# Performance work log

Hardware: AMD Instinct MI355X
Metric: run time of the kernel (lower is better)

The kernel has to match this reference:

```python
import jax, jax.numpy as jnp
import numpy as np

N = 20000      # nodes
E = 640000     # edges (before self-loops)
F = 64         # base node feature len
H = 2          # heads per layer
EPS = 1e-5
NEG_SLOPE = 0.2  # PyG GATConv leaky_relu slope


def setup_inputs():
    key = jax.random.key(0)
    ks = jax.random.split(key, 16)
    s = 0.1
    x = jax.random.normal(ks[0], (N, F), jnp.float32)
    edge_index = jax.random.randint(ks[1], (2, E), 0, N, dtype=jnp.int64)
    # layer 1: in=F, heads=H, out-per-head C1=F -> out dim H*F=128
    C1 = F
    W1 = jax.random.normal(ks[2], (F, H * C1), jnp.float32) * s
    att_src1 = jax.random.normal(ks[3], (H, C1), jnp.float32) * s
    att_dst1 = jax.random.normal(ks[4], (H, C1), jnp.float32) * s
    bias1 = jnp.zeros((H * C1,), jnp.float32)
    gamma1 = jnp.ones((H * C1,), jnp.float32)
    beta1 = jnp.zeros((H * C1,), jnp.float32)
    # layer 2: in=H*F=128, heads=H, out-per-head C2=H*F -> out dim H*H*F=256
    C2 = H * F
    W2 = jax.random.normal(ks[5], (H * C1, H * C2), jnp.float32) * s
    att_src2 = jax.random.normal(ks[6], (H, C2), jnp.float32) * s
    att_dst2 = jax.random.normal(ks[7], (H, C2), jnp.float32) * s
    bias2 = jnp.zeros((H * C2,), jnp.float32)
    gamma2 = jnp.ones((H * C2,), jnp.float32)
    beta2 = jnp.zeros((H * C2,), jnp.float32)
    return {"x": x, "edge_index": edge_index,
            "W1": W1, "att_src1": att_src1, "att_dst1": att_dst1, "bias1": bias1,
            "gamma1": gamma1, "beta1": beta1,
            "W2": W2, "att_src2": att_src2, "att_dst2": att_dst2, "bias2": bias2,
            "gamma2": gamma2, "beta2": beta2}


def _gat_conv(x, src, dst, W, att_src, att_dst, bias):
    # PyG GATConv (concat=True, add_self_loops already applied to src/dst)
    n = x.shape[0]
    h, c = att_src.shape
    hx = (x @ W).reshape(n, h, c)                       # [N,H,C]
    a_s = jnp.einsum('nhc,hc->nh', hx, att_src)         # [N,H]
    a_d = jnp.einsum('nhc,hc->nh', hx, att_dst)
    e = a_s[src] + a_d[dst]                             # [E',H]
    e = jnp.where(e > 0, e, NEG_SLOPE * e)              # leaky relu
    # segment softmax over incoming edges of each target node
    m = jax.ops.segment_max(e, dst, num_segments=n)     # [N,H]
    p = jnp.exp(e - m[dst])
    z = jax.ops.segment_sum(p, dst, num_segments=n)     # [N,H]
    alpha = p / z[dst]                                  # [E',H]
    msg = hx[src] * alpha[:, :, None]                   # [E',H,C]
    out = jax.ops.segment_sum(msg, dst, num_segments=n) # [N,H,C]
    return out.reshape(n, h * c) + bias


def _batch_norm(x, gamma, beta):
    mu = x.mean(axis=0)
    var = x.var(axis=0)  # biased, matches torch BN normalization
    return (x - mu) * jax.lax.rsqrt(var + EPS) * gamma + beta


def reference(x, edge_index, W1, att_src1, att_dst1, bias1, gamma1, beta1,
              W2, att_src2, att_dst2, bias2, gamma2, beta2):
    loops = jnp.arange(N, dtype=edge_index.dtype)
    src = jnp.concatenate([edge_index[0], loops])
    dst = jnp.concatenate([edge_index[1], loops])
    h = _gat_conv(x, src, dst, W1, att_src1, att_dst1, bias1)
    h = jax.nn.relu(_batch_norm(h, gamma1, beta1))
    h = _gat_conv(h, src, dst, W2, att_src2, att_dst2, bias2)
    h = jax.nn.relu(_batch_norm(h, gamma2, beta2))
    return h
```

## Files before the change

kernel.cpp:

```cpp
#include <hip/hip_runtime.h>
#include <hip/hip_bf16.h>
#include <math.h>

#define NN 20000
#define ER 640000
#define ET 660000
#define D1 128
#define D2 256
#define EPSV 1e-5f
#define SLOPE 0.2f
#define NT1 313
#define NHIST 64
#define HCH 10000

typedef __attribute__((ext_vector_type(8))) short bf16x8;
typedef __attribute__((ext_vector_type(4))) float f32x4;

__device__ __forceinline__ int detect64(const void* ei) {
  const int* p = (const int*)ei;
  return (p[1] | p[3] | p[5] | p[7]) == 0;
}
__device__ __forceinline__ int clampn(int v) { return v < 0 ? 0 : (v >= NN ? NN-1 : v); }
__device__ __forceinline__ float bf16_lo(unsigned int u){ return __uint_as_float(u<<16); }
__device__ __forceinline__ float bf16_hi(unsigned int u){ return __uint_as_float(u & 0xffff0000u); }

__global__ void k_hist(const void* ei, unsigned int* dpart, int* gcount) {
  extern __shared__ unsigned int hist[];
  int db = blockIdx.x, t = threadIdx.x;
  if (db == 0 && t == 0) *gcount = 0;
  for (int i = t; i < HCH; i += 256) hist[i] = 0;
  __syncthreads();
  int base = db * HCH;
  if (detect64(ei)) {
    const long long* q = (const long long*)ei + ER;
    for (int i = base + t; i < base + HCH; i += 256) {
      int d = clampn((int)q[i]);
      atomicAdd(&hist[d>>1], 1u << ((d&1)*16));
    }
  } else {
    const int* q = (const int*)ei + ER;
    for (int i = base + t; i < base + HCH; i += 256) {
      int d = clampn(q[i]);
      atomicAdd(&hist[d>>1], 1u << ((d&1)*16));
    }
  }
  __syncthreads();
  for (int i = t; i < HCH; i += 256) dpart[(size_t)db*HCH + i] = hist[i];
}

__global__ __launch_bounds__(256) void k_alloc(const unsigned int* dpart, int* begv, int* endv,
                                               int* cursor, int* gcount, float* bnz) {
  __shared__ int wsum[4], wbase[4];
  int gid = blockIdx.x*256 + threadIdx.x;
  if (gid < 768) bnz[gid] = 0.f;
  int d = 0;
  if (gid < NN) {
    d = 1;
    int half = (gid & 1) * 16;
    int idx = gid >> 1;
    for (int db = 0; db < NHIST; db++)
      d += (dpart[(size_t)db*HCH + idx] >> half) & 0xffff;
  }
  int lane = threadIdx.x & 63, w = threadIdx.x >> 6;
  int v = d;
  #pragma unroll
  for (int o = 1; o < 64; o <<= 1) {
    int u = __shfl_up(v, o);
    if (lane >= o) v += u;
  }
  if (lane == 63) wsum[w] = v;
  __syncthreads();
  if (threadIdx.x == 0) {
    int s0 = wsum[0], s1 = wsum[1], s2 = wsum[2], s3 = wsum[3];
    int b = atomicAdd(gcount, s0 + s1 + s2 + s3);
    wbase[0] = b; wbase[1] = b + s0; wbase[2] = b + s0 + s1; wbase[3] = b + s0 + s1 + s2;
  }
  __syncthreads();
  if (gid < NN) {
    int beg = wbase[w] + v - d;
    begv[gid] = beg; cursor[gid] = beg; endv[gid] = beg + d;
  }
}

__global__ __launch_bounds__(256) void k_gs(const float* x, const float* W1,
                                            const float* att_s1, const float* att_d1,
                                            __hip_bfloat16* hxb, float2* as1, float2* ad1,
                                            const void* ei, int* cursor, int* srcs) {
  __shared__ __hip_bfloat16 As[64][72];
  __shared__ __hip_bfloat16 Bs[128][72];
  __shared__ float asred[4][64], adred[4][64];
  int b = blockIdx.x, t = threadIdx.x;
  if (b >= NT1) {
    int i0 = ((b - NT1)*256 + t)*4;
    if (i0 >= ET) return;
    int s[4], d[4];
    if (i0 >= ER) {
      #pragma unroll
      for (int k = 0; k < 4; k++) { s[k] = i0 + k - ER; d[k] = s[k]; }
    } else if (detect64(ei)) {
      const long long* p64 = (const long long*)ei;
      uint4 qa = *(const uint4*)(p64 + i0);
      uint4 qb = *(const uint4*)(p64 + i0 + 2);
      uint4 ra = *(const uint4*)(p64 + ER + i0);
      uint4 rb = *(const uint4*)(p64 + ER + i0 + 2);
      s[0]=clampn((int)qa.x); s[1]=clampn((int)qa.z); s[2]=clampn((int)qb.x); s[3]=clampn((int)qb.z);
      d[0]=clampn((int)ra.x); d[1]=clampn((int)ra.z); d[2]=clampn((int)rb.x); d[3]=clampn((int)rb.z);
    } else {
      const int* p32 = (const int*)ei;
      uint4 qs = *(const uint4*)(p32 + i0);
      uint4 qd = *(const uint4*)(p32 + ER + i0);
      s[0]=clampn((int)qs.x); s[1]=clampn((int)qs.y); s[2]=clampn((int)qs.z); s[3]=clampn((int)qs.w);
      d[0]=clampn((int)qd.x); d[1]=clampn((int)qd.y); d[2]=clampn((int)qd.z); d[3]=clampn((int)qd.w);
    }
    #pragma unroll
    for (int k = 0; k < 4; k++) {
      int pos = atomicAdd(&cursor[d[k]], 1);
      srcs[pos] = s[k];
    }
    return;
  }
  int m0 = b * 64;
  for (int i = t; i < 512; i += 256) {
    int r = i >> 3, s = i & 7;
    int gr = m0 + r; if (gr >= NN) gr = NN - 1;
    float4 f0 = ((const float4*)(x + (size_t)gr*64))[s*2];
    float4 f1 = ((const float4*)(x + (size_t)gr*64))[s*2+1];
    __hip_bfloat16 hb[8] = {
      __float2bfloat16(f0.x), __float2bfloat16(f0.y), __float2bfloat16(f0.z), __float2bfloat16(f0.w),
      __float2bfloat16(f1.x), __float2bfloat16(f1.y), __float2bfloat16(f1.z), __float2bfloat16(f1.w)};
    *(uint4*)&As[r][s*8] = *(uint4*)hb;
  }
  for (int i = t; i < 8192; i += 256) {
    int n = i & 127, k = i >> 7;
    Bs[n][k] = __float2bfloat16(W1[k*128 + n]);
  }
  __syncthreads();
  int w = t >> 6, lane = t & 63, lm = lane & 15, q = lane >> 4;
  f32x4 acc[4][2];
  #pragma unroll
  for (int rt = 0; rt < 4; rt++)
    #pragma unroll
    for (int ct = 0; ct < 2; ct++) acc[rt][ct] = (f32x4){0.f,0.f,0.f,0.f};
  #pragma unroll
  for (int kc = 0; kc < 2; kc++) {
    bf16x8 bfr[2];
    #pragma unroll
    for (int ct = 0; ct < 2; ct++)
      bfr[ct] = *(const bf16x8*)&Bs[w*32 + ct*16 + lm][kc*32 + q*8];
    #pragma unroll
    for (int rt = 0; rt < 4; rt++) {
      bf16x8 a = *(const bf16x8*)&As[rt*16 + lm][kc*32 + q*8];
      acc[rt][0] = __builtin_amdgcn_mfma_f32_16x16x32_bf16(a, bfr[0], acc[rt][0], 0, 0, 0);
      acc[rt][1] = __builtin_amdgcn_mfma_f32_16x16x32_bf16(a, bfr[1], acc[rt][1], 0, 0, 0);
    }
  }
  #pragma unroll
  for (int rt = 0; rt < 4; rt++)
    #pragma unroll
    for (int ct = 0; ct < 2; ct++)
      #pragma unroll
      for (int rg = 0; rg < 4; rg++) {
        int row = m0 + rt*16 + q*4 + rg;
        int col = w*32 + ct*16 + lm;
        if (row < NN) hxb[(size_t)row*128 + col] = __float2bfloat16(acc[rt][ct][rg]);
      }
  float asc[2], adc[2];
  #pragma unroll
  for (int ct = 0; ct < 2; ct++) {
    int col = w*32 + ct*16 + lm;
    asc[ct] = att_s1[col]; adc[ct] = att_d1[col];
  }
  #pragma unroll
  for (int rt = 0; rt < 4; rt++)
    #pragma unroll
    for (int rg = 0; rg < 4; rg++) {
      float ps = acc[rt][0][rg]*asc[0] + acc[rt][1][rg]*asc[1];
      float pd = acc[rt][0][rg]*adc[0] + acc[rt][1][rg]*adc[1];
      #pragma unroll
      for (int o = 1; o < 16; o <<= 1) { ps += __shfl_xor(ps, o); pd += __shfl_xor(pd, o); }
      if (lm == 0) { int row = rt*16 + q*4 + rg; asred[w][row] = ps; adred[w][row] = pd; }
    }
  __syncthreads();
  if (t < 64) {
    int row = m0 + t;
    if (row < NN) {
      as1[row] = make_float2(asred[0][t] + asred[1][t], asred[2][t] + asred[3][t]);
      ad1[row] = make_float2(adred[0][t] + adred[1][t], adred[2][t] + adred[3][t]);
    }
  }
}

__global__ __launch_bounds__(256) void k_gemm2f(const float* out1, const float* W2,
                                                const float* bns1, const float* bnq1,
                                                const float* gamma1, const float* beta1,
                                                const float* att_s2, const float* att_d2,
                                                __hip_bfloat16* hxb, float2* as2, float2* ad2) {
  __shared__ __hip_bfloat16 As[64][136];
  __shared__ __hip_bfloat16 Bs[256][40];
  __shared__ float AB[2][128];
  __shared__ float asred[4][64], adred[4][64];
  int t = threadIdx.x;
  int m0 = blockIdx.x * 64;
  if (t < 128) {
    float mean = bns1[t]*(1.f/NN);
    float var  = bnq1[t]*(1.f/NN) - mean*mean;
    float A = rsqrtf(var + EPSV)*gamma1[t];
    AB[0][t] = A; AB[1][t] = beta1[t] - mean*A;
  }
  __syncthreads();
  for (int i = t; i < 1024; i += 256) {
    int r = i >> 4, s = i & 15;
    int gr = m0 + r; if (gr >= NN) gr = NN - 1;
    float4 f0 = ((const float4*)(out1 + (size_t)gr*128))[s*2];
    float4 f1 = ((const float4*)(out1 + (size_t)gr*128))[s*2+1];
    int c = s*8;
    float v[8] = {f0.x,f0.y,f0.z,f0.w,f1.x,f1.y,f1.z,f1.w};
    __hip_bfloat16 hb[8];
    #pragma unroll
    for (int k = 0; k < 8; k++)
      hb[k] = __float2bfloat16(fmaxf(v[k]*AB[0][c+k] + AB[1][c+k], 0.f));
    *(uint4*)&As[r][s*8] = *(uint4*)hb;
  }
  int w = t >> 6, lane = t & 63, lm = lane & 15, q = lane >> 4;
  f32x4 acc[4][4];
  #pragma unroll
  for (int rt = 0; rt < 4; rt++)
    #pragma unroll
    for (int ct = 0; ct < 4; ct++) acc[rt][ct] = (f32x4){0.f,0.f,0.f,0.f};
  for (int kc = 0; kc < 4; kc++) {
    __syncthreads();
    for (int i = t; i < 8192; i += 256) {
      int n = i & 255, kk = i >> 8;
      Bs[n][kk] = __float2bfloat16(W2[(kc*32 + kk)*256 + n]);
    }
    __syncthreads();
    bf16x8 bfr[4];
    #pragma unroll
    for (int ct = 0; ct < 4; ct++)
      bfr[ct] = *(const bf16x8*)&Bs[w*64 + ct*16 + lm][q*8];
    #pragma unroll
    for (int rt = 0; rt < 4; rt++) {
      bf16x8 a = *(const bf16x8*)&As[rt*16 + lm][kc*32 + q*8];
      #pragma unroll
      for (int ct = 0; ct < 4; ct++)
        acc[rt][ct] = __builtin_amdgcn_mfma_f32_16x16x32_bf16(a, bfr[ct], acc[rt][ct], 0, 0, 0);
    }
  }
  #pragma unroll
  for (int rt = 0; rt < 4; rt++)
    #pragma unroll
    for (int ct = 0; ct < 4; ct++)
      #pragma unroll
      for (int rg = 0; rg < 4; rg++) {
        int row = m0 + rt*16 + q*4 + rg;
        int col = w*64 + ct*16 + lm;
        if (row < NN) hxb[(size_t)row*256 + col] = __float2bfloat16(acc[rt][ct][rg]);
      }
  float asc[4], adc[4];
  #pragma unroll
  for (int ct = 0; ct < 4; ct++) {
    int col = w*64 + ct*16 + lm;
    asc[ct] = att_s2[col]; adc[ct] = att_d2[col];
  }
  #pragma unroll
  for (int rt = 0; rt < 4; rt++)
    #pragma unroll
    for (int rg = 0; rg < 4; rg++) {
      float ps = acc[rt][0][rg]*asc[0] + acc[rt][1][rg]*asc[1]
               + acc[rt][2][rg]*asc[2] + acc[rt][3][rg]*asc[3];
      float pd = acc[rt][0][rg]*adc[0] + acc[rt][1][rg]*adc[1]
               + acc[rt][2][rg]*adc[2] + acc[rt][3][rg]*adc[3];
      #pragma unroll
      for (int o = 1; o < 16; o <<= 1) { ps += __shfl_xor(ps, o); pd += __shfl_xor(pd, o); }
      if (lm == 0) { int row = rt*16 + q*4 + rg; asred[w][row] = ps; adred[w][row] = pd; }
    }
  __syncthreads();
  if (t < 64) {
    int row = m0 + t;
    if (row < NN) {
      as2[row] = make_float2(asred[0][t] + asred[1][t], asred[2][t] + asred[3][t]);
      ad2[row] = make_float2(adred[0][t] + adred[1][t], adred[2][t] + adred[3][t]);
    }
  }
}

__global__ __launch_bounds__(64) void k_agg1(const int* begv, const int* endv, const int* srcs,
                                             const float2* asv, const float2* adv,
                                             const uint4* hx, const float* bias, float* out) {
  __shared__ float2 sp[2][64];
  int n = blockIdx.x, t = threadIdx.x;
  int el = t >> 4, c = t & 15;
  int h = c >> 3;
  float2 ad = adv[n];
  int beg = begv[n], end = endv[n];
  float a[8] = {0.f,0.f,0.f,0.f,0.f,0.f,0.f,0.f};
  float z0 = 0.f, z1 = 0.f;
  for (int cb = beg; cb < end; cb += 64) {
    int len = end - cb; if (len > 64) len = 64;
    if (t < len) {
      int s = srcs[cb + t];
      float2 as = asv[s];
      float e0 = as.x + ad.x, e1 = as.y + ad.y;
      e0 = e0 > 0.f ? e0 : SLOPE*e0;
      e1 = e1 > 0.f ? e1 : SLOPE*e1;
      float p0 = __expf(e0), p1 = __expf(e1);
      sp[0][t] = make_float2(__int_as_float(s), p0);
      sp[1][t] = make_float2(__int_as_float(s), p1);
      z0 += p0; z1 += p1;
    }
    __syncthreads();
    for (int j = 0; j < len; j += 4) {
      int e = j + el;
      if (e < len) {
        float2 v = sp[h][e];
        uint4 u = hx[(size_t)__float_as_int(v.x)*16 + c];
        float pj = v.y;
        a[0] += pj*bf16_lo(u.x); a[1] += pj*bf16_hi(u.x);
        a[2] += pj*bf16_lo(u.y); a[3] += pj*bf16_hi(u.y);
        a[4] += pj*bf16_lo(u.z); a[5] += pj*bf16_hi(u.z);
        a[6] += pj*bf16_lo(u.w); a[7] += pj*bf16_hi(u.w);
      }
    }
    __syncthreads();
  }
  #pragma unroll
  for (int k = 0; k < 8; k++) {
    a[k] += __shfl_down(a[k], 32);
    a[k] += __shfl_down(a[k], 16);
  }
  #pragma unroll
  for (int o = 1; o < 64; o <<= 1) { z0 += __shfl_xor(z0, o); z1 += __shfl_xor(z1, o); }
  if (t < 16) {
    float inv = 1.f / (h ? z1 : z0);
    float4 b0 = ((const float4*)bias)[2*c];
    float4 b1 = ((const float4*)bias)[2*c+1];
    float4 o0 = { a[0]*inv + b0.x, a[1]*inv + b0.y, a[2]*inv + b0.z, a[3]*inv + b0.w };
    float4 o1 = { a[4]*inv + b1.x, a[5]*inv + b1.y, a[6]*inv + b1.z, a[7]*inv + b1.w };
    ((float4*)(out + (size_t)n*D1))[2*c]   = o0;
    ((float4*)(out + (size_t)n*D1))[2*c+1] = o1;
  }
}

__global__ __launch_bounds__(64) void k_agg2(const int* begv, const int* endv, const int* srcs,
                                             const float2* asv, const float2* adv,
                                             const uint4* hx, const float* bias, float* out) {
  __shared__ float2 sp[2][64];
  int n = blockIdx.x, t = threadIdx.x;
  int el = t >> 5, c = t & 31;
  int h = c >> 4;
  float2 ad = adv[n];
  int beg = begv[n], end = endv[n];
  float a[8] = {0.f,0.f,0.f,0.f,0.f,0.f,0.f,0.f};
  float z0 = 0.f, z1 = 0.f;
  for (int cb = beg; cb < end; cb += 64) {
    int len = end - cb; if (len > 64) len = 64;
    if (t < len) {
      int s = srcs[cb + t];
      float2 as = asv[s];
      float e0 = as.x + ad.x, e1 = as.y + ad.y;
      e0 = e0 > 0.f ? e0 : SLOPE*e0;
      e1 = e1 > 0.f ? e1 : SLOPE*e1;
      float p0 = __expf(e0), p1 = __expf(e1);
      sp[0][t] = make_float2(__int_as_float(s), p0);
      sp[1][t] = make_float2(__int_as_float(s), p1);
      z0 += p0; z1 += p1;
    }
    __syncthreads();
    for (int j = 0; j < len; j += 2) {
      int e = j + el;
      if (e < len) {
        float2 v = sp[h][e];
        uint4 u = hx[(size_t)__float_as_int(v.x)*32 + c];
        float pj = v.y;
        a[0] += pj*bf16_lo(u.x); a[1] += pj*bf16_hi(u.x);
        a[2] += pj*bf16_lo(u.y); a[3] += pj*bf16_hi(u.y);
        a[4] += pj*bf16_lo(u.z); a[5] += pj*bf16_hi(u.z);
        a[6] += pj*bf16_lo(u.w); a[7] += pj*bf16_hi(u.w);
      }
    }
    __syncthreads();
  }
  #pragma unroll
  for (int k = 0; k < 8; k++) a[k] += __shfl_down(a[k], 32);
  #pragma unroll
  for (int o = 1; o < 64; o <<= 1) { z0 += __shfl_xor(z0, o); z1 += __shfl_xor(z1, o); }
  if (t < 32) {
    float inv = 1.f / (h ? z1 : z0);
    float4 b0 = ((const float4*)bias)[2*c];
    float4 b1 = ((const float4*)bias)[2*c+1];
    float4 o0 = { a[0]*inv + b0.x, a[1]*inv + b0.y, a[2]*inv + b0.z, a[3]*inv + b0.w };
    float4 o1 = { a[4]*inv + b1.x, a[5]*inv + b1.y, a[6]*inv + b1.z, a[7]*inv + b1.w };
    ((float4*)(out + (size_t)n*D2))[2*c]   = o0;
    ((float4*)(out + (size_t)n*D2))[2*c+1] = o1;
  }
}

template<int D>
__global__ void k_bnstats(const float* x, float* bnsum, float* bnsq) {
  const int ROWS = 100;
  int c = threadIdx.x;
  int r0 = blockIdx.x * ROWS;
  float s = 0.f, s2 = 0.f;
  for (int r = 0; r < ROWS; r++) {
    float v = x[(size_t)(r0 + r)*D + c];
    s += v; s2 += v*v;
  }
  atomicAdd(&bnsum[c], s);
  atomicAdd(&bnsq[c], s2);
}

__global__ void k_bnapply2(const float* x, const float* bnsum, const float* bnsq,
                           const float* gamma, const float* beta, float* out) {
  int i = blockIdx.x*blockDim.x + threadIdx.x;
  if (i >= NN*D2/4) return;
  int c = (i & 63) * 4;
  float4 v = ((const float4*)x)[i];
  float r[4] = {v.x, v.y, v.z, v.w};
  #pragma unroll
  for (int k = 0; k < 4; k++) {
    float mean = bnsum[c+k] * (1.f/NN);
    float var  = bnsq[c+k] * (1.f/NN) - mean*mean;
    float o = (r[k] - mean) * rsqrtf(var + EPSV) * gamma[c+k] + beta[c+k];
    r[k] = o > 0.f ? o : 0.f;
  }
  float4 o4 = {r[0], r[1], r[2], r[3]};
  ((float4*)out)[i] = o4;
}

extern "C" void kernel_launch(void* const* d_in, const int* in_sizes, int n_in,
                              void* d_out, int out_size, void* d_ws, size_t ws_size,
                              hipStream_t stream) {
  const float* x      = (const float*)d_in[0];
  const void*  ei     = d_in[1];
  const float* W1     = (const float*)d_in[2];
  const float* att_s1 = (const float*)d_in[3];
  const float* att_d1 = (const float*)d_in[4];
  const float* bias1  = (const float*)d_in[5];
  const float* gamma1 = (const float*)d_in[6];
  const float* beta1  = (const float*)d_in[7];
  const float* W2     = (const float*)d_in[8];
  const float* att_s2 = (const float*)d_in[9];
  const float* att_d2 = (const float*)d_in[10];
  const float* bias2  = (const float*)d_in[11];
  const float* gamma2 = (const float*)d_in[12];
  const float* beta2  = (const float*)d_in[13];

  char* p = (char*)d_ws;
  __hip_bfloat16* hx1b = (__hip_bfloat16*)p; p += (size_t)NN*D1*2;
  __hip_bfloat16* hx2b = (__hip_bfloat16*)p; p += (size_t)NN*D2*2;
  float* out1 = (float*)p; p += (size_t)NN*D1*4;
  float* out2 = (float*)p; p += (size_t)NN*D2*4;
  float2* as1 = (float2*)p; p += (size_t)NN*8;
  float2* ad1 = (float2*)p; p += (size_t)NN*8;
  float2* as2 = (float2*)p; p += (size_t)NN*8;
  float2* ad2 = (float2*)p; p += (size_t)NN*8;
  float* bns1 = (float*)p; p += D1*4;
  float* bnq1 = (float*)p; p += D1*4;
  float* bns2 = (float*)p; p += D2*4;
  float* bnq2 = (float*)p; p += D2*4;
  unsigned int* dpart = (unsigned int*)p; p += (size_t)NHIST*HCH*4;
  int* begv   = (int*)p; p += NN*4;
  int* endv   = (int*)p; p += NN*4;
  int* cursor = (int*)p; p += NN*4;
  int* gcount = (int*)p; p += 16*4;
  int* srcs   = (int*)p; p += (size_t)ET*4;

  const int SCB = (ET/4 + 255)/256;
  k_hist<<<NHIST, 256, HCH*4, stream>>>(ei, dpart, gcount);
  k_alloc<<<(NN+255)/256, 256, 0, stream>>>(dpart, begv, endv, cursor, gcount, bns1);
  k_gs<<<NT1 + SCB, 256, 0, stream>>>(x, W1, att_s1, att_d1, hx1b, as1, ad1,
                                      ei, cursor, srcs);

  k_agg1<<<NN, 64, 0, stream>>>(begv, endv, srcs, as1, ad1, (const uint4*)hx1b, bias1, out1);
  k_bnstats<D1><<<200, D1, 0, stream>>>(out1, bns1, bnq1);

  k_gemm2f<<<(NN+63)/64, 256, 0, stream>>>(out1, W2, bns1, bnq1, gamma1, beta1,
                                           att_s2, att_d2, hx2b, as2, ad2);
  k_agg2<<<NN, 64, 0, stream>>>(begv, endv, srcs, as2, ad2, (const uint4*)hx2b, bias2, out2);
  k_bnstats<D2><<<200, D2, 0, stream>>>(out2, bns2, bnq2);
  k_bnapply2<<<(NN*D2/4 + 255)/256, 256, 0, stream>>>(out2, bns2, bnq2, gamma2, beta2,
                                                      (float*)d_out);
}
```

Baseline: 254.3 us.

## Fuse BatchNorm statistics into persistent multi-wave aggregation kernels

Both aggregation kernels are reorganised into persistent 256-thread blocks. Each of the four waves in a block handles one destination node at a time in a grid-stride loop, and block-wide barriers become wave barriers. Per-channel sum and sum-of-squares for BatchNorm are gathered in shared memory with shared atomics, then flushed once per block to global memory. This removes the two separate k_bnstats kernels, their launches and their re-read of the aggregation outputs. The cost is shared-memory atomic traffic on every node and a fixed grid of 2048 blocks.

Result: slower. 344.1 us (+35.3%).

```diff
diff --git a/kernel.cpp b/kernel.cpp
--- a/kernel.cpp
+++ b/kernel.cpp
@@ -12,6 +12,7 @@
 #define NT1 313
 #define NHIST 64
 #define HCH 10000
+#define AGB 2048
 
 typedef __attribute__((ext_vector_type(8))) short bf16x8;
 typedef __attribute__((ext_vector_type(4))) float f32x4;
@@ -284,129 +285,144 @@
   }
 }
 
-__global__ __launch_bounds__(64) void k_agg1(const int* begv, const int* endv, const int* srcs,
-                                             const float2* asv, const float2* adv,
-                                             const uint4* hx, const float* bias, float* out) {
-  __shared__ float2 sp[2][64];
-  int n = blockIdx.x, t = threadIdx.x;
-  int el = t >> 4, c = t & 15;
-  int h = c >> 3;
-  float2 ad = adv[n];
-  int beg = begv[n], end = endv[n];
-  float a[8] = {0.f,0.f,0.f,0.f,0.f,0.f,0.f,0.f};
-  float z0 = 0.f, z1 = 0.f;
-  for (int cb = beg; cb < end; cb += 64) {
-    int len = end - cb; if (len > 64) len = 64;
-    if (t < len) {
-      int s = srcs[cb + t];
-      float2 as = asv[s];
-      float e0 = as.x + ad.x, e1 = as.y + ad.y;
-      e0 = e0 > 0.f ? e0 : SLOPE*e0;
-      e1 = e1 > 0.f ? e1 : SLOPE*e1;
-      float p0 = __expf(e0), p1 = __expf(e1);
-      sp[0][t] = make_float2(__int_as_float(s), p0);
-      sp[1][t] = make_float2(__int_as_float(s), p1);
-      z0 += p0; z1 += p1;
-    }
-    __syncthreads();
-    for (int j = 0; j < len; j += 4) {
-      int e = j + el;
-      if (e < len) {
-        float2 v = sp[h][e];
-        uint4 u = hx[(size_t)__float_as_int(v.x)*16 + c];
-        float pj = v.y;
-        a[0] += pj*bf16_lo(u.x); a[1] += pj*bf16_hi(u.x);
-        a[2] += pj*bf16_lo(u.y); a[3] += pj*bf16_hi(u.y);
-        a[4] += pj*bf16_lo(u.z); a[5] += pj*bf16_hi(u.z);
-        a[6] += pj*bf16_lo(u.w); a[7] += pj*bf16_hi(u.w);
-      }
-    }
-    __syncthreads();
-  }
-  #pragma unroll
-  for (int k = 0; k < 8; k++) {
-    a[k] += __shfl_down(a[k], 32);
-    a[k] += __shfl_down(a[k], 16);
-  }
-  #pragma unroll
-  for (int o = 1; o < 64; o <<= 1) { z0 += __shfl_xor(z0, o); z1 += __shfl_xor(z1, o); }
-  if (t < 16) {
-    float inv = 1.f / (h ? z1 : z0);
-    float4 b0 = ((const float4*)bias)[2*c];
-    float4 b1 = ((const float4*)bias)[2*c+1];
-    float4 o0 = { a[0]*inv + b0.x, a[1]*inv + b0.y, a[2]*inv + b0.z, a[3]*inv + b0.w };
-    float4 o1 = { a[4]*inv + b1.x, a[5]*inv + b1.y, a[6]*inv + b1.z, a[7]*inv + b1.w };
-    ((float4*)(out + (size_t)n*D1))[2*c]   = o0;
-    ((float4*)(out + (size_t)n*D1))[2*c+1] = o1;
-  }
-}
-
-__global__ __launch_bounds__(64) void k_agg2(const int* begv, const int* endv, const int* srcs,
-                                             const float2* asv, const float2* adv,
-                                             const uint4* hx, const float* bias, float* out) {
-  __shared__ float2 sp[2][64];
-  int n = blockIdx.x, t = threadIdx.x;
-  int el = t >> 5, c = t & 31;
-  int h = c >> 4;
-  float2 ad = adv[n];
-  int beg = begv[n], end = endv[n];
-  float a[8] = {0.f,0.f,0.f,0.f,0.f,0.f,0.f,0.f};
-  float z0 = 0.f, z1 = 0.f;
-  for (int cb = beg; cb < end; cb += 64) {
-    int len = end - cb; if (len > 64) len = 64;
-    if (t < len) {
-      int s = srcs[cb + t];
-      float2 as = asv[s];
-      float e0 = as.x + ad.x, e1 = as.y + ad.y;
-      e0 = e0 > 0.f ? e0 : SLOPE*e0;
-      e1 = e1 > 0.f ? e1 : SLOPE*e1;
-      float p0 = __expf(e0), p1 = __expf(e1);
-      sp[0][t] = make_float2(__int_as_float(s), p0);
-      sp[1][t] = make_float2(__int_as_float(s), p1);
-      z0 += p0; z1 += p1;
-    }
-    __syncthreads();
-    for (int j = 0; j < len; j += 2) {
-      int e = j + el;
-      if (e < len) {
-        float2 v = sp[h][e];
-        uint4 u = hx[(size_t)__float_as_int(v.x)*32 + c];
-        float pj = v.y;
-        a[0] += pj*bf16_lo(u.x); a[1] += pj*bf16_hi(u.x);
-        a[2] += pj*bf16_lo(u.y); a[3] += pj*bf16_hi(u.y);
-        a[4] += pj*bf16_lo(u.z); a[5] += pj*bf16_hi(u.z);
-        a[6] += pj*bf16_lo(u.w); a[7] += pj*bf16_hi(u.w);
-      }
-    }
-    __syncthreads();
-  }
-  #pragma unroll
-  for (int k = 0; k < 8; k++) a[k] += __shfl_down(a[k], 32);
-  #pragma unroll
-  for (int o = 1; o < 64; o <<= 1) { z0 += __shfl_xor(z0, o); z1 += __shfl_xor(z1, o); }
-  if (t < 32) {
-    float inv = 1.f / (h ? z1 : z0);
-    float4 b0 = ((const float4*)bias)[2*c];
-    float4 b1 = ((const float4*)bias)[2*c+1];
-    float4 o0 = { a[0]*inv + b0.x, a[1]*inv + b0.y, a[2]*inv + b0.z, a[3]*inv + b0.w };
-    float4 o1 = { a[4]*inv + b1.x, a[5]*inv + b1.y, a[6]*inv + b1.z, a[7]*inv + b1.w };
-    ((float4*)(out + (size_t)n*D2))[2*c]   = o0;
-    ((float4*)(out + (size_t)n*D2))[2*c+1] = o1;
-  }
-}
-
-template<int D>
-__global__ void k_bnstats(const float* x, float* bnsum, float* bnsq) {
-  const int ROWS = 100;
-  int c = threadIdx.x;
-  int r0 = blockIdx.x * ROWS;
-  float s = 0.f, s2 = 0.f;
-  for (int r = 0; r < ROWS; r++) {
-    float v = x[(size_t)(r0 + r)*D + c];
-    s += v; s2 += v*v;
-  }
-  atomicAdd(&bnsum[c], s);
-  atomicAdd(&bnsq[c], s2);
+__global__ __launch_bounds__(256) void k_agg1s(const int* begv, const int* endv, const int* srcs,
+                                               const float2* asv, const float2* adv,
+                                               const uint4* hx, const float* bias,
+                                               float* out, float* bn ) {
+  __shared__ float2 sp[4][2][64];
+  __shared__ float bnacc[256];
+  int t = threadIdx.x;
+  bnacc[t] = 0.f;
+  __syncthreads();
+  int wid = t >> 6, lane = t & 63;
+  int el = lane >> 4, c = lane & 15, h = c >> 3;
+  for (int n = blockIdx.x*4 + wid; n < NN; n += AGB*4) {
+    float2 ad = adv[n];
+    int beg = begv[n], end = endv[n];
+    float a[8] = {0.f,0.f,0.f,0.f,0.f,0.f,0.f,0.f};
+    float z0 = 0.f, z1 = 0.f;
+    for (int cb = beg; cb < end; cb += 64) {
+      int len = end - cb; if (len > 64) len = 64;
+      if (lane < len) {
+        int s = srcs[cb + lane];
+        float2 as = asv[s];
+        float e0 = as.x + ad.x, e1 = as.y + ad.y;
+        e0 = e0 > 0.f ? e0 : SLOPE*e0;
+        e1 = e1 > 0.f ? e1 : SLOPE*e1;
+        float p0 = __expf(e0), p1 = __expf(e1);
+        sp[wid][0][lane] = make_float2(__int_as_float(s), p0);
+        sp[wid][1][lane] = make_float2(__int_as_float(s), p1);
+        z0 += p0; z1 += p1;
+      }
+      __builtin_amdgcn_wave_barrier();
+      for (int j = 0; j < len; j += 4) {
+        int e = j + el;
+        if (e < len) {
+          float2 v = sp[wid][h][e];
+          uint4 u = hx[(size_t)__float_as_int(v.x)*16 + c];
+          float pj = v.y;
+          a[0] += pj*bf16_lo(u.x); a[1] += pj*bf16_hi(u.x);
+          a[2] += pj*bf16_lo(u.y); a[3] += pj*bf16_hi(u.y);
+          a[4] += pj*bf16_lo(u.z); a[5] += pj*bf16_hi(u.z);
+          a[6] += pj*bf16_lo(u.w); a[7] += pj*bf16_hi(u.w);
+        }
+      }
+      __builtin_amdgcn_wave_barrier();
+    }
+    #pragma unroll
+    for (int k = 0; k < 8; k++) {
+      a[k] += __shfl_down(a[k], 32);
+      a[k] += __shfl_down(a[k], 16);
+    }
+    #pragma unroll
+    for (int o = 1; o < 64; o <<= 1) { z0 += __shfl_xor(z0, o); z1 += __shfl_xor(z1, o); }
+    if (lane < 16) {
+      float inv = 1.f / (h ? z1 : z0);
+      float4 b0 = ((const float4*)bias)[2*c];
+      float4 b1 = ((const float4*)bias)[2*c+1];
+      float4 o0 = { a[0]*inv + b0.x, a[1]*inv + b0.y, a[2]*inv + b0.z, a[3]*inv + b0.w };
+      float4 o1 = { a[4]*inv + b1.x, a[5]*inv + b1.y, a[6]*inv + b1.z, a[7]*inv + b1.w };
+      ((float4*)(out + (size_t)n*D1))[2*c]   = o0;
+      ((float4*)(out + (size_t)n*D1))[2*c+1] = o1;
+      float vv[8] = {o0.x,o0.y,o0.z,o0.w,o1.x,o1.y,o1.z,o1.w};
+      #pragma unroll
+      for (int k = 0; k < 8; k++) {
+        atomicAdd(&bnacc[8*c+k], vv[k]);
+        atomicAdd(&bnacc[128+8*c+k], vv[k]*vv[k]);
+      }
+    }
+  }
+  __syncthreads();
+  atomicAdd(&bn[t], bnacc[t]);
+}
+
+__global__ __launch_bounds__(256) void k_agg2s(const int* begv, const int* endv, const int* srcs,
+                                               const float2* asv, const float2* adv,
+                                               const uint4* hx, const float* bias,
+                                               float* out, float* bn ) {
+  __shared__ float2 sp[4][2][64];
+  __shared__ float bnacc[512];
+  int t = threadIdx.x;
+  bnacc[t] = 0.f; bnacc[256+t] = 0.f;
+  __syncthreads();
+  int wid = t >> 6, lane = t & 63;
+  int el = lane >> 5, c = lane & 31, h = c >> 4;
+  for (int n = blockIdx.x*4 + wid; n < NN; n += AGB*4) {
+    float2 ad = adv[n];
+    int beg = begv[n], end = endv[n];
+    float a[8] = {0.f,0.f,0.f,0.f,0.f,0.f,0.f,0.f};
+    float z0 = 0.f, z1 = 0.f;
+    for (int cb = beg; cb < end; cb += 64) {
+      int len = end - cb; if (len > 64) len = 64;
+      if (lane < len) {
+        int s = srcs[cb + lane];
+        float2 as = asv[s];
+        float e0 = as.x + ad.x, e1 = as.y + ad.y;
+        e0 = e0 > 0.f ? e0 : SLOPE*e0;
+        e1 = e1 > 0.f ? e1 : SLOPE*e1;
+        float p0 = __expf(e0), p1 = __expf(e1);
+        sp[wid][0][lane] = make_float2(__int_as_float(s), p0);
+        sp[wid][1][lane] = make_float2(__int_as_float(s), p1);
+        z0 += p0; z1 += p1;
+      }
+      __builtin_amdgcn_wave_barrier();
+      for (int j = 0; j < len; j += 2) {
+        int e = j + el;
+        if (e < len) {
+          float2 v = sp[wid][h][e];
+          uint4 u = hx[(size_t)__float_as_int(v.x)*32 + c];
+          float pj = v.y;
+          a[0] += pj*bf16_lo(u.x); a[1] += pj*bf16_hi(u.x);
+          a[2] += pj*bf16_lo(u.y); a[3] += pj*bf16_hi(u.y);
+          a[4] += pj*bf16_lo(u.z); a[5] += pj*bf16_hi(u.z);
+          a[6] += pj*bf16_lo(u.w); a[7] += pj*bf16_hi(u.w);
+        }
+      }
+      __builtin_amdgcn_wave_barrier();
+    }
+    #pragma unroll
+    for (int k = 0; k < 8; k++) a[k] += __shfl_down(a[k], 32);
+    #pragma unroll
+    for (int o = 1; o < 64; o <<= 1) { z0 += __shfl_xor(z0, o); z1 += __shfl_xor(z1, o); }
+    if (lane < 32) {
+      float inv = 1.f / (h ? z1 : z0);
+      float4 b0 = ((const float4*)bias)[2*c];
+      float4 b1 = ((const float4*)bias)[2*c+1];
+      float4 o0 = { a[0]*inv + b0.x, a[1]*inv + b0.y, a[2]*inv + b0.z, a[3]*inv + b0.w };
+      float4 o1 = { a[4]*inv + b1.x, a[5]*inv + b1.y, a[6]*inv + b1.z, a[7]*inv + b1.w };
+      ((float4*)(out + (size_t)n*D2))[2*c]   = o0;
+      ((float4*)(out + (size_t)n*D2))[2*c+1] = o1;
+      float vv[8] = {o0.x,o0.y,o0.z,o0.w,o1.x,o1.y,o1.z,o1.w};
+      #pragma unroll
+      for (int k = 0; k < 8; k++) {
+        atomicAdd(&bnacc[8*c+k], vv[k]);
+        atomicAdd(&bnacc[256+8*c+k], vv[k]*vv[k]);
+      }
+    }
+  }
+  __syncthreads();
+  atomicAdd(&bn[t], bnacc[t]);
+  atomicAdd(&bn[256+t], bnacc[256+t]);
 }
 
 __global__ void k_bnapply2(const float* x, const float* bnsum, const float* bnsq,
@@ -454,10 +470,8 @@
   float2* ad1 = (float2*)p; p += (size_t)NN*8;
   float2* as2 = (float2*)p; p += (size_t)NN*8;
   float2* ad2 = (float2*)p; p += (size_t)NN*8;
-  float* bns1 = (float*)p; p += D1*4;
-  float* bnq1 = (float*)p; p += D1*4;
-  float* bns2 = (float*)p; p += D2*4;
-  float* bnq2 = (float*)p; p += D2*4;
+  float* bn1  = (float*)p; p += 256*4;
+  float* bn2  = (float*)p; p += 512*4;
   unsigned int* dpart = (unsigned int*)p; p += (size_t)NHIST*HCH*4;
   int* begv   = (int*)p; p += NN*4;
   int* endv   = (int*)p; p += NN*4;
@@ -467,17 +481,16 @@
 
   const int SCB = (ET/4 + 255)/256;
   k_hist<<<NHIST, 256, HCH*4, stream>>>(ei, dpart, gcount);
-  k_alloc<<<(NN+255)/256, 256, 0, stream>>>(dpart, begv, endv, cursor, gcount, bns1);
+  k_alloc<<<(NN+255)/256, 256, 0, stream>>>(dpart, begv, endv, cursor, gcount, bn1);
   k_gs<<<NT1 + SCB, 256, 0, stream>>>(x, W1, att_s1, att_d1, hx1b, as1, ad1,
                                       ei, cursor, srcs);
 
-  k_agg1<<<NN, 64, 0, stream>>>(begv, endv, srcs, as1, ad1, (const uint4*)hx1b, bias1, out1);
-  k_bnstats<D1><<<200, D1, 0, stream>>>(out1, bns1, bnq1);
-
-  k_gemm2f<<<(NN+63)/64, 256, 0, stream>>>(out1, W2, bns1, bnq1, gamma1, beta1,
+  k_agg1s<<<AGB, 256, 0, stream>>>(begv, endv, srcs, as1, ad1, (const uint4*)hx1b,
+                                   bias1, out1, bn1);
+  k_gemm2f<<<(NN+63)/64, 256, 0, stream>>>(out1, W2, bn1, bn1+128, gamma1, beta1,
                                            att_s2, att_d2, hx2b, as2, ad2);
-  k_agg2<<<NN, 64, 0, stream>>>(begv, endv, srcs, as2, ad2, (const uint4*)hx2b, bias2, out2);
-  k_bnstats<D2><<<200, D2, 0, stream>>>(out2, bns2, bnq2);
-  k_bnapply2<<<(NN*D2/4 + 255)/256, 256, 0, stream>>>(out2, bns2, bnq2, gamma2, beta2,
+  k_agg2s<<<AGB, 256, 0, stream>>>(begv, endv, srcs, as2, ad2, (const uint4*)hx2b,
+                                   bias2, out2, bn2);
+  k_bnapply2<<<(NN*D2/4 + 255)/256, 256, 0, stream>>>(out2, bn2, bn2+256, gamma2, beta2,
                                                       (float*)d_out);
 }
```

## Fuse BN statistics into consumers using grid-wide atomic barriers

Applied to the files above, without the earlier changes.

The separate batch-norm statistics kernels are removed. For layer 1, each GEMM2 block now accumulates column sums over its own 64 rows. For layer 2, a single kernel computes the statistics and then applies the normalisation and ReLU. Both kernels wait on an atomic counter acting as a software grid barrier, which cuts three launches and one extra pass over the data. The risk is deadlock if not all 313 or 200 blocks are co-resident. The counters sit in the zero-initialised region of the workspace, which grows from 768 to 784 floats so they are cleared each run.

After: 334.1 us. 31.4% more time.

```diff
diff --git a/kernel.cpp b/kernel.cpp
--- a/kernel.cpp
+++ b/kernel.cpp
@@ -12,6 +12,7 @@
 #define NT1 313
 #define NHIST 64
 #define HCH 10000
+#define BN2B 200
 
 typedef __attribute__((ext_vector_type(8))) short bf16x8;
 typedef __attribute__((ext_vector_type(4))) float f32x4;
@@ -52,7 +53,7 @@
                                                int* cursor, int* gcount, float* bnz) {
   __shared__ int wsum[4], wbase[4];
   int gid = blockIdx.x*256 + threadIdx.x;
-  if (gid < 768) bnz[gid] = 0.f;
+  if (gid < 784) bnz[gid] = 0.f;
   int d = 0;
   if (gid < NN) {
     d = 1;
@@ -190,11 +191,11 @@
   }
 }
 
-__global__ __launch_bounds__(256) void k_gemm2f(const float* out1, const float* W2,
-                                                const float* bns1, const float* bnq1,
-                                                const float* gamma1, const float* beta1,
-                                                const float* att_s2, const float* att_d2,
-                                                __hip_bfloat16* hxb, float2* as2, float2* ad2) {
+__global__ __launch_bounds__(256, 2) void k_gemm2f(const float* out1, const float* W2,
+                                                   float* bns1, float* bnq1, int* cnt,
+                                                   const float* gamma1, const float* beta1,
+                                                   const float* att_s2, const float* att_d2,
+                                                   __hip_bfloat16* hxb, float2* as2, float2* ad2) {
   __shared__ __hip_bfloat16 As[64][136];
   __shared__ __hip_bfloat16 Bs[256][40];
   __shared__ float AB[2][128];
@@ -202,8 +203,25 @@
   int t = threadIdx.x;
   int m0 = blockIdx.x * 64;
   if (t < 128) {
-    float mean = bns1[t]*(1.f/NN);
-    float var  = bnq1[t]*(1.f/NN) - mean*mean;
+    float s = 0.f, s2 = 0.f;
+    for (int r = 0; r < 64; r++) {
+      int row = m0 + r;
+      if (row < NN) { float v = out1[(size_t)row*128 + t]; s += v; s2 += v*v; }
+    }
+    atomicAdd(&bns1[t], s); atomicAdd(&bnq1[t], s2);
+  }
+  __threadfence();
+  __syncthreads();
+  if (t == 0) {
+    atomicAdd(cnt, 1);
+    while (atomicAdd(cnt, 0) < NT1) __builtin_amdgcn_s_sleep(10);
+  }
+  __syncthreads();
+  if (t < 128) {
+    float sum = atomicAdd(&bns1[t], 0.f);
+    float sq  = atomicAdd(&bnq1[t], 0.f);
+    float mean = sum*(1.f/NN);
+    float var  = sq*(1.f/NN) - mean*mean;
     float A = rsqrtf(var + EPSV)*gamma1[t];
     AB[0][t] = A; AB[1][t] = beta1[t] - mean*A;
   }
@@ -395,36 +413,37 @@
   }
 }
 
-template<int D>
-__global__ void k_bnstats(const float* x, float* bnsum, float* bnsq) {
+__global__ __launch_bounds__(256) void k_bn2(const float* x, float* bnsum, float* bnsq,
+                                             int* cnt, const float* gamma, const float* beta,
+                                             float* out) {
   const int ROWS = 100;
   int c = threadIdx.x;
   int r0 = blockIdx.x * ROWS;
   float s = 0.f, s2 = 0.f;
   for (int r = 0; r < ROWS; r++) {
-    float v = x[(size_t)(r0 + r)*D + c];
+    float v = x[(size_t)(r0 + r)*D2 + c];
     s += v; s2 += v*v;
   }
   atomicAdd(&bnsum[c], s);
   atomicAdd(&bnsq[c], s2);
-}
-
-__global__ void k_bnapply2(const float* x, const float* bnsum, const float* bnsq,
-                           const float* gamma, const float* beta, float* out) {
-  int i = blockIdx.x*blockDim.x + threadIdx.x;
-  if (i >= NN*D2/4) return;
-  int c = (i & 63) * 4;
-  float4 v = ((const float4*)x)[i];
-  float r[4] = {v.x, v.y, v.z, v.w};
-  #pragma unroll
-  for (int k = 0; k < 4; k++) {
-    float mean = bnsum[c+k] * (1.f/NN);
-    float var  = bnsq[c+k] * (1.f/NN) - mean*mean;
-    float o = (r[k] - mean) * rsqrtf(var + EPSV) * gamma[c+k] + beta[c+k];
-    r[k] = o > 0.f ? o : 0.f;
-  }
-  float4 o4 = {r[0], r[1], r[2], r[3]};
-  ((float4*)out)[i] = o4;
+  __threadfence();
+  __syncthreads();
+  if (c == 0) {
+    atomicAdd(cnt, 1);
+    while (atomicAdd(cnt, 0) < BN2B) __builtin_amdgcn_s_sleep(10);
+  }
+  __syncthreads();
+  float sum = atomicAdd(&bnsum[c], 0.f);
+  float sq  = atomicAdd(&bnsq[c], 0.f);
+  float mean = sum*(1.f/NN);
+  float var  = sq*(1.f/NN) - mean*mean;
+  float A = rsqrtf(var + EPSV)*gamma[c];
+  float B = beta[c] - mean*A;
+  for (int r = 0; r < ROWS; r++) {
+    float v = x[(size_t)(r0 + r)*D2 + c];
+    float o = v*A + B;
+    out[(size_t)(r0 + r)*D2 + c] = o > 0.f ? o : 0.f;
+  }
 }
 
 extern "C" void kernel_launch(void* const* d_in, const int* in_sizes, int n_in,
@@ -458,6 +477,7 @@
   float* bnq1 = (float*)p; p += D1*4;
   float* bns2 = (float*)p; p += D2*4;
   float* bnq2 = (float*)p; p += D2*4;
+  int* cnt_g2 = (int*)p;  p += 16*4;
   unsigned int* dpart = (unsigned int*)p; p += (size_t)NHIST*HCH*4;
   int* begv   = (int*)p; p += NN*4;
   int* endv   = (int*)p; p += NN*4;
@@ -472,12 +492,8 @@
                                       ei, cursor, srcs);
 
   k_agg1<<<NN, 64, 0, stream>>>(begv, endv, srcs, as1, ad1, (const uint4*)hx1b, bias1, out1);
-  k_bnstats<D1><<<200, D1, 0, stream>>>(out1, bns1, bnq1);
-
-  k_gemm2f<<<(NN+63)/64, 256, 0, stream>>>(out1, W2, bns1, bnq1, gamma1, beta1,
-                                           att_s2, att_d2, hx2b, as2, ad2);
+  k_gemm2f<<<NT1, 256, 0, stream>>>(out1, W2, bns1, bnq1, cnt_g2, gamma1, beta1,
+                                    att_s2, att_d2, hx2b, as2, ad2);
   k_agg2<<<NN, 64, 0, stream>>>(begv, endv, srcs, as2, ad2, (const uint4*)hx2b, bias2, out2);
-  k_bnstats<D2><<<200, D2, 0, stream>>>(out2, bns2, bnq2);
-  k_bnapply2<<<(NN*D2/4 + 255)/256, 256, 0, stream>>>(out2, bns2, bnq2, gamma2, beta2,
-                                                      (float*)d_out);
-}
+  k_bn2<<<BN2B, 256, 0, stream>>>(out2, bns2, bnq2, cnt_g2 + 1, gamma2, beta2, (float*)d_out);
+}
```
